# Performance work log

Hardware: AMD Instinct MI355X
Metric: run time of the kernel (lower is better)

Reference implementation:

```python
import jax, jax.numpy as jnp
import numpy as np

B, S, D, H = 2, 2048, 1024, 16
DK = D // H
LN_EPS = 1e-5


def setup_inputs() -> dict:
    key = jax.random.key(0)
    ks = jax.random.split(key, 10)
    scale = 1.0 / np.sqrt(D)
    return {
        "input_Q": jax.random.normal(ks[0], (B, S, D), jnp.float32),
        "input_K": jax.random.normal(ks[1], (B, S, D), jnp.float32),
        "input_V": jax.random.normal(ks[2], (B, S, D), jnp.float32),
        "mask": jax.random.randint(ks[3], (B, S, S), 0, 2, jnp.int32),
        "W_Q": jax.random.normal(ks[4], (D, D), jnp.float32) * scale,
        "W_K": jax.random.normal(ks[5], (D, D), jnp.float32) * scale,
        "W_V": jax.random.normal(ks[6], (D, D), jnp.float32) * scale,
        "W_O": jax.random.normal(ks[7], (D, D), jnp.float32) * scale,
        "ln_gamma": jnp.ones((D,), jnp.float32),
        "ln_beta": jnp.zeros((D,), jnp.float32),
    }


def reference(input_Q, input_K, input_V, mask, W_Q, W_K, W_V, W_O, ln_gamma, ln_beta):
    # projections -> [B, H, S, DK]
    q = (input_Q @ W_Q).reshape(B, S, H, DK).transpose(0, 2, 1, 3)
    k = (input_K @ W_K).reshape(B, S, H, DK).transpose(0, 2, 1, 3)
    v = (input_V @ W_V).reshape(B, S, H, DK).transpose(0, 2, 1, 3)

    # explicit O(S^2) scores as in the original module
    scores = jnp.einsum("bhqd,bhkd->bhqk", q, k) / np.sqrt(DK)
    scores = jnp.where(mask[:, None, :, :].astype(bool), -1e9, scores)
    attn = jax.nn.softmax(scores, axis=-1)
    ctx = jnp.einsum("bhqk,bhkd->bhqd", attn, v)

    # merge heads, output projection, residual + LayerNorm
    ctx = ctx.transpose(0, 2, 1, 3).reshape(B, S, D)
    out = ctx @ W_O + input_Q
    mu = out.mean(-1, keepdims=True)
    var = jnp.mean((out - mu) ** 2, -1, keepdims=True)
    return (out - mu) * jax.lax.rsqrt(var + LN_EPS) * ln_gamma + ln_beta
```

## Files before the change

### kernel.cpp

```cpp
#include <hip/hip_runtime.h>

typedef __bf16 bf16x8 __attribute__((ext_vector_type(8)));
typedef float  f32x4  __attribute__((ext_vector_type(4)));

#define AS1 __attribute__((address_space(1)))
#define AS3 __attribute__((address_space(3)))

__device__ __forceinline__ void g2l16(const void* g, void* l) {
  __builtin_amdgcn_global_load_lds((AS1 void*)g, (AS3 void*)l, 16, 0, 0);
}
#define MFMA16(a, b, c) __builtin_amdgcn_mfma_f32_16x16x32_bf16(a, b, c, 0, 0, 0)

__device__ __forceinline__ unsigned pack_bf16(float a, float b) {
  union { __bf16 h[2]; unsigned u; } p;
  p.h[0] = (__bf16)a; p.h[1] = (__bf16)b;
  return p.u;
}

__global__ __launch_bounds__(256) void prep(const float* __restrict__ inQ,
    const float* __restrict__ inK, const float* __restrict__ inV,
    const int* __restrict__ mask,
    const float* __restrict__ W0, const float* __restrict__ W1,
    const float* __restrict__ W2, const float* __restrict__ W3,
    __bf16* __restrict__ Xq, __bf16* __restrict__ Xk, __bf16* __restrict__ Xv,
    unsigned long long* __restrict__ bits, __bf16* __restrict__ Wt) {
  __shared__ __bf16 tile[64][65];
  const int blk = blockIdx.x;
  if (blk < 6144) {
    const int z = blk >> 11, bx = blk & 2047;
    const float* src = z == 0 ? inQ : (z == 1 ? inK : inV);
    __bf16* dst = z == 0 ? Xq : (z == 1 ? Xk : Xv);
    size_t base = ((size_t)bx * 256 + threadIdx.x) * 8;
    float4 f0 = *(const float4*)(src + base);
    float4 f1 = *(const float4*)(src + base + 4);
    bf16x8 o;
    o[0] = (__bf16)f0.x; o[1] = (__bf16)f0.y; o[2] = (__bf16)f0.z; o[3] = (__bf16)f0.w;
    o[4] = (__bf16)f1.x; o[5] = (__bf16)f1.y; o[6] = (__bf16)f1.z; o[7] = (__bf16)f1.w;
    *(bf16x8*)(dst + base) = o;
  } else if (blk < 10240) {
    const int lane = threadIdx.x & 63, w = threadIdx.x >> 6;
    const int base = (blk - 6144) * 2048 + w * 512;
#pragma unroll
    for (int it = 0; it < 8; ++it) {
      int i = base + it * 64 + lane;
      unsigned long long bb = __ballot(mask[i] != 0);
      if (lane == 0) bits[i >> 6] = bb;
    }
  } else {
    const int idx = blk - 10240;
    const int z = idx >> 8, rem = idx & 255, bx = rem & 15, by = rem >> 4;
    const float* srcs[4] = {W0, W1, W2, W3};
    const float* src = srcs[z];
    __bf16* dst = Wt + (size_t)z * 1024 * 1024;
    int cb = bx * 64, rb = by * 64;
    for (int i = threadIdx.x; i < 4096; i += 256) {
      int r = i >> 6, c = i & 63;
      tile[r][c] = (__bf16)src[(size_t)(rb + r) * 1024 + cb + c];
    }
    __syncthreads();
    for (int i = threadIdx.x; i < 4096; i += 256) {
      int c = i >> 6, r = i & 63;
      dst[(size_t)(cb + c) * 1024 + rb + r] = tile[r][c];
    }
  }
}

__global__ __launch_bounds__(256) void qkv_gemm(const __bf16* __restrict__ Xq,
    const __bf16* __restrict__ Xk, const __bf16* __restrict__ Xv,
    const __bf16* __restrict__ Wt, __bf16* __restrict__ Qb,
    __bf16* __restrict__ Kb, __bf16* __restrict__ Vtb) {
  __shared__ __align__(16) __bf16 sh[8192];
  __bf16* As = sh;
  __bf16* Bs = sh + 4096;
  const int z = blockIdx.z;
  const __bf16* X = z == 0 ? Xq : (z == 1 ? Xk : Xv);
  const __bf16* W = Wt + (size_t)z * 1048576;
  const float scale = z == 0 ? 0.125f * 1.44269504088896f : 1.f;
  const int t = threadIdx.x;
  const int lane = t & 63, w = t >> 6;
  const int lane15 = lane & 15, quad = lane >> 4;
  const int wm = (w >> 1) * 64, wn = (w & 1) * 64;
  const int mBase = blockIdx.y * 128, nBase = blockIdx.x * 128;
  const int c1 = t, c2 = t + 256;
  f32x4 acc[4][4] = {};
  for (int kt = 0; kt < 1024; kt += 32) {
    __syncthreads();
    g2l16(X + (size_t)(mBase + (c1 >> 2)) * 1024 + kt + (c1 & 3) * 8, As + c1 * 8);
    g2l16(X + (size_t)(mBase + (c2 >> 2)) * 1024 + kt + (c2 & 3) * 8, As + c2 * 8);
    g2l16(W + (size_t)(nBase + (c1 >> 2)) * 1024 + kt + (c1 & 3) * 8, Bs + c1 * 8);
    g2l16(W + (size_t)(nBase + (c2 >> 2)) * 1024 + kt + (c2 & 3) * 8, Bs + c2 * 8);
    __builtin_amdgcn_s_waitcnt(0);
    __syncthreads();
    bf16x8 a[4], b[4];
#pragma unroll
    for (int i = 0; i < 4; i++) a[i] = *(const bf16x8*)&As[(wm + i * 16 + lane15) * 32 + quad * 8];
#pragma unroll
    for (int j = 0; j < 4; j++) b[j] = *(const bf16x8*)&Bs[(wn + j * 16 + lane15) * 32 + quad * 8];
#pragma unroll
    for (int i = 0; i < 4; i++)
#pragma unroll
      for (int j = 0; j < 4; j++)
        acc[i][j] = MFMA16(a[i], b[j], acc[i][j]);
  }
  if (z != 2) {
    __bf16* Y = z == 0 ? Qb : Kb;
#pragma unroll
    for (int i = 0; i < 4; i++)
#pragma unroll
      for (int j = 0; j < 4; j++)
#pragma unroll
        for (int r = 0; r < 4; r++) {
          int mg = mBase + wm + i * 16 + quad * 4 + r;
          int ng = nBase + wn + j * 16 + lane15;
          int b_ = mg >> 11, s_ = mg & 2047, h_ = ng >> 6, d_ = ng & 63;
          Y[(((size_t)(b_ * 16 + h_)) * 2048 + s_) * 64 + d_] = (__bf16)(acc[i][j][r] * scale);
        }
  } else {
    const int s0 = mBase & 2047;
    const int bhBase = (mBase >> 11) * 16 + (nBase >> 6);
#pragma unroll
    for (int half = 0; half < 2; ++half) {
      __syncthreads();
      if ((w & 1) == half) {
#pragma unroll
        for (int i = 0; i < 4; i++)
#pragma unroll
          for (int j = 0; j < 4; j++)
#pragma unroll
            for (int r = 0; r < 4; r++) {
              int nl = j * 16 + lane15;
              int ml = wm + i * 16 + quad * 4 + r;
              sh[nl * 128 + (ml ^ ((nl & 7) * 16))] = (__bf16)acc[i][j][r];
            }
      }
      __syncthreads();
      const int row = t >> 2, c0 = (t & 3) * 32;
      const int xr = (row & 7) * 16;
      const int b0 = row * 128 + (c0 ^ xr);
      const int b1 = row * 128 + ((c0 + 16) ^ xr);
      bf16x8 a0 = *(const bf16x8*)&sh[b0];
      bf16x8 a1 = *(const bf16x8*)&sh[b0 + 8];
      bf16x8 a2 = *(const bf16x8*)&sh[b1];
      bf16x8 a3 = *(const bf16x8*)&sh[b1 + 8];
      __bf16* dst = Vtb + (size_t)(bhBase + half) * 131072 + (size_t)row * 2048 + s0 + c0;
      *(bf16x8*)(dst)      = a0;
      *(bf16x8*)(dst + 8)  = a1;
      *(bf16x8*)(dst + 16) = a2;
      *(bf16x8*)(dst + 24) = a3;
    }
  }
}

__global__ __launch_bounds__(256) void gemm_wo(const __bf16* __restrict__ X,
    const __bf16* __restrict__ Wt, const float* __restrict__ resid,
    float* __restrict__ Yf) {
  __shared__ __align__(16) __bf16 As[128 * 32];
  __shared__ __align__(16) __bf16 Bs[128 * 32];
  const int t = threadIdx.x;
  const int lane = t & 63, w = t >> 6;
  const int lane15 = lane & 15, quad = lane >> 4;
  const int wm = (w >> 1) * 64, wn = (w & 1) * 64;
  const int mBase = blockIdx.y * 128, nBase = blockIdx.x * 128;
  const int c1 = t, c2 = t + 256;
  f32x4 acc[4][4] = {};
  for (int kt = 0; kt < 1024; kt += 32) {
    __syncthreads();
    g2l16(X  + (size_t)(mBase + (c1 >> 2)) * 1024 + kt + (c1 & 3) * 8, As + c1 * 8);
    g2l16(X  + (size_t)(mBase + (c2 >> 2)) * 1024 + kt + (c2 & 3) * 8, As + c2 * 8);
    g2l16(Wt + (size_t)(nBase + (c1 >> 2)) * 1024 + kt + (c1 & 3) * 8, Bs + c1 * 8);
    g2l16(Wt + (size_t)(nBase + (c2 >> 2)) * 1024 + kt + (c2 & 3) * 8, Bs + c2 * 8);
    __builtin_amdgcn_s_waitcnt(0);
    __syncthreads();
    bf16x8 a[4], b[4];
#pragma unroll
    for (int i = 0; i < 4; i++) a[i] = *(const bf16x8*)&As[(wm + i * 16 + lane15) * 32 + quad * 8];
#pragma unroll
    for (int j = 0; j < 4; j++) b[j] = *(const bf16x8*)&Bs[(wn + j * 16 + lane15) * 32 + quad * 8];
#pragma unroll
    for (int i = 0; i < 4; i++)
#pragma unroll
      for (int j = 0; j < 4; j++)
        acc[i][j] = MFMA16(a[i], b[j], acc[i][j]);
  }
#pragma unroll
  for (int i = 0; i < 4; i++)
#pragma unroll
    for (int j = 0; j < 4; j++)
#pragma unroll
      for (int r = 0; r < 4; r++) {
        int mg = mBase + wm + i * 16 + quad * 4 + r;
        int ng = nBase + wn + j * 16 + lane15;
        size_t idx = (size_t)mg * 1024 + ng;
        Yf[idx] = acc[i][j][r] + resid[idx];
      }
}

__global__ __launch_bounds__(256) void attn_kernel(const __bf16* __restrict__ Q,
    const __bf16* __restrict__ Kp, const __bf16* __restrict__ Vt,
    const unsigned* __restrict__ mbits, __bf16* __restrict__ ctx) {
  __shared__ __align__(16) __bf16 Qs[64 * 64];
  __shared__ __align__(16) __bf16 Ks[2][32 * 64];
  __shared__ __align__(16) __bf16 Vs[2][64 * 32];
  __shared__ __align__(16) __bf16 Ps[4][16 * 32];
  const int t = threadIdx.x, lane = t & 63, w = t >> 6;
  const int l15 = lane & 15, quad = lane >> 4;
  const int bh = blockIdx.y, b = bh >> 4, h = bh & 15;
  const int qBase = blockIdx.x * 64;
  const size_t qko = (size_t)bh * 2048 * 64;
  const size_t vko = (size_t)bh * 64 * 2048;
  const int srow8 = lane >> 3, sch8 = (lane & 7) ^ srow8;
  const int srow16 = lane >> 2, sch4 = (lane & 3) ^ (srow16 & 3);
  g2l16(Q + qko + (size_t)(qBase + w * 8 + srow8) * 64 + sch8 * 8,       Qs + w * 512 + lane * 8);
  g2l16(Q + qko + (size_t)(qBase + (w + 4) * 8 + srow8) * 64 + sch8 * 8, Qs + (w + 4) * 512 + lane * 8);
  g2l16(Kp + qko + (size_t)(w * 8 + srow8) * 64 + sch8 * 8,   &Ks[0][0] + w * 512 + lane * 8);
  g2l16(Vt + vko + (size_t)(w * 16 + srow16) * 2048 + sch4 * 8, &Vs[0][0] + w * 512 + lane * 8);
  __builtin_amdgcn_s_waitcnt(0);
  __syncthreads();
  bf16x8 qb0, qb1;
  {
    const int r = w * 16 + l15, s = r & 7;
    qb0 = *(const bf16x8*)&Qs[r * 64 + ((quad ^ s) * 8)];
    qb1 = *(const bf16x8*)&Qs[r * 64 + (((4 + quad) ^ s) * 8)];
  }
  bf16x8 ones;
#pragma unroll
  for (int i = 0; i < 8; i++) ones[i] = (__bf16)1.0f;
  f32x4 o[4] = {};
  f32x4 ol = {};
  const size_t mIdx = ((size_t)b * 2048 + qBase + w * 16 + l15) * 64;
  unsigned m32 = mbits[mIdx];
  int cur = 0;
  for (int kt = 0; kt < 64; ++kt) {
    __syncthreads();
    unsigned mnext = 0;
    if (kt < 63) {
      const int tB = (kt + 1) * 32, nb = cur ^ 1;
      g2l16(Kp + qko + (size_t)(tB + w * 8 + srow8) * 64 + sch8 * 8,        &Ks[nb][0] + w * 512 + lane * 8);
      g2l16(Vt + vko + (size_t)(w * 16 + srow16) * 2048 + tB + sch4 * 8,    &Vs[nb][0] + w * 512 + lane * 8);
      mnext = mbits[mIdx + kt + 1];
    }
    f32x4 st[2];
#pragma unroll
    for (int j = 0; j < 2; j++) {
      const int tr = j * 16 + l15, s = tr & 7;
      bf16x8 ka0 = *(const bf16x8*)&Ks[cur][tr * 64 + ((quad ^ s) * 8)];
      bf16x8 ka1 = *(const bf16x8*)&Ks[cur][tr * 64 + (((4 + quad) ^ s) * 8)];
      f32x4 zz = {0.f, 0.f, 0.f, 0.f};
      zz = MFMA16(ka0, qb0, zz);
      st[j] = MFMA16(ka1, qb1, zz);
    }
#pragma unroll
    for (int j = 0; j < 2; j++) {
      const int t0 = j * 16 + quad * 4;
      float e0 = ((m32 >> (t0 + 0)) & 1u) ? 0.f : __builtin_exp2f(st[j][0]);
      float e1 = ((m32 >> (t0 + 1)) & 1u) ? 0.f : __builtin_exp2f(st[j][1]);
      float e2 = ((m32 >> (t0 + 2)) & 1u) ? 0.f : __builtin_exp2f(st[j][2]);
      float e3 = ((m32 >> (t0 + 3)) & 1u) ? 0.f : __builtin_exp2f(st[j][3]);
      const int ch = t0 >> 3;
      char* pbase = (char*)&Ps[w][0] + l15 * 64 + ((ch ^ (l15 & 3)) * 16) + ((t0 & 7) * 2);
      *(unsigned*)(pbase)     = pack_bf16(e0, e1);
      *(unsigned*)(pbase + 4) = pack_bf16(e2, e3);
    }
    m32 = mnext;
    __builtin_amdgcn_s_waitcnt(0xC07F);
    bf16x8 pa = *(const bf16x8*)&Ps[w][l15 * 32 + ((quad ^ (l15 & 3)) * 8)];
    ol = MFMA16(pa, ones, ol);
#pragma unroll
    for (int j = 0; j < 4; j++) {
      const int dr = j * 16 + l15;
      bf16x8 vb = *(const bf16x8*)&Vs[cur][dr * 32 + ((quad ^ (dr & 3)) * 8)];
      o[j] = MFMA16(pa, vb, o[j]);
    }
    cur ^= 1;
  }
#pragma unroll
  for (int r = 0; r < 4; r++) {
    float inv = 1.f / ol[r];
    int qg = qBase + w * 16 + quad * 4 + r;
    size_t base = ((size_t)b * 2048 + qg) * 1024 + h * 64;
#pragma unroll
    for (int j = 0; j < 4; j++)
      ctx[base + j * 16 + l15] = (__bf16)(o[j][r] * inv);
  }
}

__global__ __launch_bounds__(256) void ln_kernel(const float* __restrict__ X,
    const float* __restrict__ gamma, const float* __restrict__ beta,
    float* __restrict__ out) {
  __shared__ float red[8];
  const int t = threadIdx.x;
  const size_t row = blockIdx.x;
  const float* xr = X + row * 1024;
  float4 x = *(const float4*)(xr + t * 4);
  float s = x.x + x.y + x.z + x.w;
  float s2 = x.x * x.x + x.y * x.y + x.z * x.z + x.w * x.w;
#pragma unroll
  for (int off = 1; off < 64; off <<= 1) { s += __shfl_xor(s, off); s2 += __shfl_xor(s2, off); }
  if ((t & 63) == 0) { red[t >> 6] = s; red[4 + (t >> 6)] = s2; }
  __syncthreads();
  float S1 = red[0] + red[1] + red[2] + red[3];
  float S2 = red[4] + red[5] + red[6] + red[7];
  float mu = S1 * (1.f / 1024.f);
  float var = S2 * (1.f / 1024.f) - mu * mu;
  float rs = rsqrtf(var + 1e-5f);
  float4 g = *(const float4*)(gamma + t * 4);
  float4 bb = *(const float4*)(beta + t * 4);
  float4 y;
  y.x = (x.x - mu) * rs * g.x + bb.x;
  y.y = (x.y - mu) * rs * g.y + bb.y;
  y.z = (x.z - mu) * rs * g.z + bb.z;
  y.w = (x.w - mu) * rs * g.w + bb.w;
  *(float4*)(out + row * 1024 + t * 4) = y;
}

extern "C" void kernel_launch(void* const* d_in, const int* in_sizes, int n_in,
                              void* d_out, int out_size, void* d_ws, size_t ws_size,
                              hipStream_t stream) {
  const float* inQ  = (const float*)d_in[0];
  const float* inK  = (const float*)d_in[1];
  const float* inV  = (const float*)d_in[2];
  const int*   mask = (const int*)d_in[3];
  const float* WQ   = (const float*)d_in[4];
  const float* WK   = (const float*)d_in[5];
  const float* WV   = (const float*)d_in[6];
  const float* WO   = (const float*)d_in[7];
  const float* gamma = (const float*)d_in[8];
  const float* beta  = (const float*)d_in[9];

  const size_t MB = 1024 * 1024;
  char* ws = (char*)d_ws;
  __bf16* Xq  = (__bf16*)(ws);
  __bf16* Xk  = (__bf16*)(ws + 8 * MB);
  __bf16* Xv  = (__bf16*)(ws + 16 * MB);
  __bf16* Qb  = (__bf16*)(ws + 24 * MB);
  __bf16* Kb  = (__bf16*)(ws + 32 * MB);
  __bf16* Vtb = (__bf16*)(ws + 48 * MB);
  __bf16* Wt  = (__bf16*)(ws + 56 * MB);
  unsigned long long* mbits = (unsigned long long*)(ws + 64 * MB);
  __bf16* ctx  = Xq;
  float*  outp = (float*)(ws + 8 * MB);

  prep<<<dim3(11264), 256, 0, stream>>>(inQ, inK, inV, mask, WQ, WK, WV, WO,
                                        Xq, Xk, Xv, mbits, Wt);
  qkv_gemm<<<dim3(8, 32, 3), 256, 0, stream>>>(Xq, Xk, Xv, Wt, Qb, Kb, Vtb);
  attn_kernel<<<dim3(32, 32), 256, 0, stream>>>(Qb, Kb, Vtb, (const unsigned*)mbits, ctx);
  gemm_wo<<<dim3(8, 32), 256, 0, stream>>>(ctx, Wt + 3 * 1048576, inQ, outp);
  ln_kernel<<<dim3(4096), 256, 0, stream>>>(outp, gamma, beta, (float*)d_out);
}
```

Baseline: 317.1 us.

## Use additive float mask in attention, retile Wo GEMM, adjust LDS swizzles

The prep kernel now expands the int mask into a float additive mask (0 or -1e9) instead of a packed bitmask. Attention adds it to scores before exp2, removing per-element bit tests and selects. gemm_wo moves to 64x128 tiles for twice as many blocks, and the V and P LDS swizzles change to reduce bank conflicts. The float mask costs much more memory traffic than the bitmask, per head and in prep.

Measured after the change: 316.3 us. Within noise of the previous version (-0.3%).

```diff
diff --git a/kernel.cpp b/kernel.cpp
--- a/kernel.cpp
+++ b/kernel.cpp
@@ -23,7 +23,7 @@
     const float* __restrict__ W0, const float* __restrict__ W1,
     const float* __restrict__ W2, const float* __restrict__ W3,
     __bf16* __restrict__ Xq, __bf16* __restrict__ Xk, __bf16* __restrict__ Xv,
-    unsigned long long* __restrict__ bits, __bf16* __restrict__ Wt) {
+    float* __restrict__ Mf, __bf16* __restrict__ Wt) {
   __shared__ __bf16 tile[64][65];
   const int blk = blockIdx.x;
   if (blk < 6144) {
@@ -38,14 +38,16 @@
     o[4] = (__bf16)f1.x; o[5] = (__bf16)f1.y; o[6] = (__bf16)f1.z; o[7] = (__bf16)f1.w;
     *(bf16x8*)(dst + base) = o;
   } else if (blk < 10240) {
-    const int lane = threadIdx.x & 63, w = threadIdx.x >> 6;
-    const int base = (blk - 6144) * 2048 + w * 512;
-#pragma unroll
-    for (int it = 0; it < 8; ++it) {
-      int i = base + it * 64 + lane;
-      unsigned long long bb = __ballot(mask[i] != 0);
-      if (lane == 0) bits[i >> 6] = bb;
-    }
+    size_t base = ((size_t)(blk - 6144) * 2048) + (size_t)threadIdx.x * 8;
+    int4 m0 = *(const int4*)(mask + base);
+    int4 m1 = *(const int4*)(mask + base + 4);
+    float4 f0, f1;
+    f0.x = m0.x ? -1e9f : 0.f; f0.y = m0.y ? -1e9f : 0.f;
+    f0.z = m0.z ? -1e9f : 0.f; f0.w = m0.w ? -1e9f : 0.f;
+    f1.x = m1.x ? -1e9f : 0.f; f1.y = m1.y ? -1e9f : 0.f;
+    f1.z = m1.z ? -1e9f : 0.f; f1.w = m1.w ? -1e9f : 0.f;
+    *(float4*)(Mf + base) = f0;
+    *(float4*)(Mf + base + 4) = f1;
   } else {
     const int idx = blk - 10240;
     const int z = idx >> 8, rem = idx & 255, bx = rem & 15, by = rem >> 4;
@@ -154,36 +156,34 @@
 __global__ __launch_bounds__(256) void gemm_wo(const __bf16* __restrict__ X,
     const __bf16* __restrict__ Wt, const float* __restrict__ resid,
     float* __restrict__ Yf) {
-  __shared__ __align__(16) __bf16 As[128 * 32];
+  __shared__ __align__(16) __bf16 As[64 * 32];
   __shared__ __align__(16) __bf16 Bs[128 * 32];
   const int t = threadIdx.x;
   const int lane = t & 63, w = t >> 6;
   const int lane15 = lane & 15, quad = lane >> 4;
-  const int wm = (w >> 1) * 64, wn = (w & 1) * 64;
-  const int mBase = blockIdx.y * 128, nBase = blockIdx.x * 128;
-  const int c1 = t, c2 = t + 256;
-  f32x4 acc[4][4] = {};
+  const int wm = (w >> 1) * 32, wn = (w & 1) * 64;
+  const int mBase = blockIdx.y * 64, nBase = blockIdx.x * 128;
+  f32x4 acc[2][4] = {};
   for (int kt = 0; kt < 1024; kt += 32) {
     __syncthreads();
-    g2l16(X  + (size_t)(mBase + (c1 >> 2)) * 1024 + kt + (c1 & 3) * 8, As + c1 * 8);
-    g2l16(X  + (size_t)(mBase + (c2 >> 2)) * 1024 + kt + (c2 & 3) * 8, As + c2 * 8);
-    g2l16(Wt + (size_t)(nBase + (c1 >> 2)) * 1024 + kt + (c1 & 3) * 8, Bs + c1 * 8);
-    g2l16(Wt + (size_t)(nBase + (c2 >> 2)) * 1024 + kt + (c2 & 3) * 8, Bs + c2 * 8);
+    g2l16(X  + (size_t)(mBase + (t >> 2)) * 1024 + kt + (t & 3) * 8, As + t * 8);
+    g2l16(Wt + (size_t)(nBase + (t >> 2)) * 1024 + kt + (t & 3) * 8, Bs + t * 8);
+    g2l16(Wt + (size_t)(nBase + ((t + 256) >> 2)) * 1024 + kt + (t & 3) * 8, Bs + (t + 256) * 8);
     __builtin_amdgcn_s_waitcnt(0);
     __syncthreads();
-    bf16x8 a[4], b[4];
-#pragma unroll
-    for (int i = 0; i < 4; i++) a[i] = *(const bf16x8*)&As[(wm + i * 16 + lane15) * 32 + quad * 8];
+    bf16x8 a[2], b[4];
+#pragma unroll
+    for (int i = 0; i < 2; i++) a[i] = *(const bf16x8*)&As[(wm + i * 16 + lane15) * 32 + quad * 8];
 #pragma unroll
     for (int j = 0; j < 4; j++) b[j] = *(const bf16x8*)&Bs[(wn + j * 16 + lane15) * 32 + quad * 8];
 #pragma unroll
-    for (int i = 0; i < 4; i++)
+    for (int i = 0; i < 2; i++)
 #pragma unroll
       for (int j = 0; j < 4; j++)
         acc[i][j] = MFMA16(a[i], b[j], acc[i][j]);
   }
 #pragma unroll
-  for (int i = 0; i < 4; i++)
+  for (int i = 0; i < 2; i++)
 #pragma unroll
     for (int j = 0; j < 4; j++)
 #pragma unroll
@@ -197,7 +197,7 @@
 
 __global__ __launch_bounds__(256) void attn_kernel(const __bf16* __restrict__ Q,
     const __bf16* __restrict__ Kp, const __bf16* __restrict__ Vt,
-    const unsigned* __restrict__ mbits, __bf16* __restrict__ ctx) {
+    const float* __restrict__ Mf, __bf16* __restrict__ ctx) {
   __shared__ __align__(16) __bf16 Qs[64 * 64];
   __shared__ __align__(16) __bf16 Ks[2][32 * 64];
   __shared__ __align__(16) __bf16 Vs[2][64 * 32];
@@ -209,11 +209,15 @@
   const size_t qko = (size_t)bh * 2048 * 64;
   const size_t vko = (size_t)bh * 64 * 2048;
   const int srow8 = lane >> 3, sch8 = (lane & 7) ^ srow8;
-  const int srow16 = lane >> 2, sch4 = (lane & 3) ^ (srow16 & 3);
+  const int srow16 = lane >> 2, sch4 = (lane & 3) ^ ((lane >> 3) & 3);
+  const int psw = (l15 >> 1) & 3;
   g2l16(Q + qko + (size_t)(qBase + w * 8 + srow8) * 64 + sch8 * 8,       Qs + w * 512 + lane * 8);
   g2l16(Q + qko + (size_t)(qBase + (w + 4) * 8 + srow8) * 64 + sch8 * 8, Qs + (w + 4) * 512 + lane * 8);
-  g2l16(Kp + qko + (size_t)(w * 8 + srow8) * 64 + sch8 * 8,   &Ks[0][0] + w * 512 + lane * 8);
+  g2l16(Kp + qko + (size_t)(w * 8 + srow8) * 64 + sch8 * 8,     &Ks[0][0] + w * 512 + lane * 8);
   g2l16(Vt + vko + (size_t)(w * 16 + srow16) * 2048 + sch4 * 8, &Vs[0][0] + w * 512 + lane * 8);
+  const float* Mrow = Mf + ((size_t)b * 2048 + qBase + w * 16 + l15) * 2048 + quad * 4;
+  float4 mc0 = *(const float4*)(Mrow);
+  float4 mc1 = *(const float4*)(Mrow + 16);
   __builtin_amdgcn_s_waitcnt(0);
   __syncthreads();
   bf16x8 qb0, qb1;
@@ -227,17 +231,16 @@
   for (int i = 0; i < 8; i++) ones[i] = (__bf16)1.0f;
   f32x4 o[4] = {};
   f32x4 ol = {};
-  const size_t mIdx = ((size_t)b * 2048 + qBase + w * 16 + l15) * 64;
-  unsigned m32 = mbits[mIdx];
   int cur = 0;
   for (int kt = 0; kt < 64; ++kt) {
     __syncthreads();
-    unsigned mnext = 0;
+    float4 mn0, mn1;
     if (kt < 63) {
       const int tB = (kt + 1) * 32, nb = cur ^ 1;
-      g2l16(Kp + qko + (size_t)(tB + w * 8 + srow8) * 64 + sch8 * 8,        &Ks[nb][0] + w * 512 + lane * 8);
-      g2l16(Vt + vko + (size_t)(w * 16 + srow16) * 2048 + tB + sch4 * 8,    &Vs[nb][0] + w * 512 + lane * 8);
-      mnext = mbits[mIdx + kt + 1];
+      g2l16(Kp + qko + (size_t)(tB + w * 8 + srow8) * 64 + sch8 * 8,     &Ks[nb][0] + w * 512 + lane * 8);
+      g2l16(Vt + vko + (size_t)(w * 16 + srow16) * 2048 + tB + sch4 * 8, &Vs[nb][0] + w * 512 + lane * 8);
+      mn0 = *(const float4*)(Mrow + tB);
+      mn1 = *(const float4*)(Mrow + tB + 16);
     }
     f32x4 st[2];
 #pragma unroll
@@ -251,24 +254,25 @@
     }
 #pragma unroll
     for (int j = 0; j < 2; j++) {
+      const float4 mv = j == 0 ? mc0 : mc1;
+      float e0 = __builtin_exp2f(st[j][0] + mv.x);
+      float e1 = __builtin_exp2f(st[j][1] + mv.y);
+      float e2 = __builtin_exp2f(st[j][2] + mv.z);
+      float e3 = __builtin_exp2f(st[j][3] + mv.w);
       const int t0 = j * 16 + quad * 4;
-      float e0 = ((m32 >> (t0 + 0)) & 1u) ? 0.f : __builtin_exp2f(st[j][0]);
-      float e1 = ((m32 >> (t0 + 1)) & 1u) ? 0.f : __builtin_exp2f(st[j][1]);
-      float e2 = ((m32 >> (t0 + 2)) & 1u) ? 0.f : __builtin_exp2f(st[j][2]);
-      float e3 = ((m32 >> (t0 + 3)) & 1u) ? 0.f : __builtin_exp2f(st[j][3]);
       const int ch = t0 >> 3;
-      char* pbase = (char*)&Ps[w][0] + l15 * 64 + ((ch ^ (l15 & 3)) * 16) + ((t0 & 7) * 2);
+      char* pbase = (char*)&Ps[w][0] + l15 * 64 + ((ch ^ psw) * 16) + ((t0 & 7) * 2);
       *(unsigned*)(pbase)     = pack_bf16(e0, e1);
       *(unsigned*)(pbase + 4) = pack_bf16(e2, e3);
     }
-    m32 = mnext;
+    mc0 = mn0; mc1 = mn1;
     __builtin_amdgcn_s_waitcnt(0xC07F);
-    bf16x8 pa = *(const bf16x8*)&Ps[w][l15 * 32 + ((quad ^ (l15 & 3)) * 8)];
+    bf16x8 pa = *(const bf16x8*)&Ps[w][l15 * 32 + ((quad ^ psw) * 8)];
     ol = MFMA16(pa, ones, ol);
 #pragma unroll
     for (int j = 0; j < 4; j++) {
       const int dr = j * 16 + l15;
-      bf16x8 vb = *(const bf16x8*)&Vs[cur][dr * 32 + ((quad ^ (dr & 3)) * 8)];
+      bf16x8 vb = *(const bf16x8*)&Vs[cur][dr * 32 + ((quad ^ ((dr >> 1) & 3)) * 8)];
       o[j] = MFMA16(pa, vb, o[j]);
     }
     cur ^= 1;
@@ -336,14 +340,14 @@
   __bf16* Kb  = (__bf16*)(ws + 32 * MB);
   __bf16* Vtb = (__bf16*)(ws + 48 * MB);
   __bf16* Wt  = (__bf16*)(ws + 56 * MB);
-  unsigned long long* mbits = (unsigned long long*)(ws + 64 * MB);
+  float*  Mf  = (float*)(ws + 66 * MB);
   __bf16* ctx  = Xq;
   float*  outp = (float*)(ws + 8 * MB);
 
   prep<<<dim3(11264), 256, 0, stream>>>(inQ, inK, inV, mask, WQ, WK, WV, WO,
-                                        Xq, Xk, Xv, mbits, Wt);
+                                        Xq, Xk, Xv, Mf, Wt);
   qkv_gemm<<<dim3(8, 32, 3), 256, 0, stream>>>(Xq, Xk, Xv, Wt, Qb, Kb, Vtb);
-  attn_kernel<<<dim3(32, 32), 256, 0, stream>>>(Qb, Kb, Vtb, (const unsigned*)mbits, ctx);
-  gemm_wo<<<dim3(8, 32), 256, 0, stream>>>(ctx, Wt + 3 * 1048576, inQ, outp);
+  attn_kernel<<<dim3(32, 32), 256, 0, stream>>>(Qb, Kb, Vtb, Mf, ctx);
+  gemm_wo<<<dim3(8, 64), 256, 0, stream>>>(ctx, Wt + 3 * 1048576, inQ, outp);
   ln_kernel<<<dim3(4096), 256, 0, stream>>>(outp, gamma, beta, (float*)d_out);
 }
```

## Software-pipeline attention PV stage and halve output-projection GEMM M-tile

Applied to the files above, without the earlier changes.

The attention loop now defers each tile's P·V MFMAs by one iteration, so the QK^T MFMAs of tile kt overlap with the P·V of tile kt-1. To support this it uses a 4-deep V buffer and a double-buffered P scratch per wave, and changes the LDS swizzle for V and P. Separately, gemm_wo drops to 64x128 tiles and launches twice as many blocks, which gives 512 blocks across the CUs but less reuse of the B tile. The extra LDS may lower attention occupancy, and the new swizzles have to stay consistent between writer and reader.

Result: faster. 308.4 us (-2.8%).

```diff
diff --git a/kernel.cpp b/kernel.cpp
--- a/kernel.cpp
+++ b/kernel.cpp
@@ -154,36 +154,34 @@
 __global__ __launch_bounds__(256) void gemm_wo(const __bf16* __restrict__ X,
     const __bf16* __restrict__ Wt, const float* __restrict__ resid,
     float* __restrict__ Yf) {
-  __shared__ __align__(16) __bf16 As[128 * 32];
+  __shared__ __align__(16) __bf16 As[64 * 32];
   __shared__ __align__(16) __bf16 Bs[128 * 32];
   const int t = threadIdx.x;
   const int lane = t & 63, w = t >> 6;
   const int lane15 = lane & 15, quad = lane >> 4;
-  const int wm = (w >> 1) * 64, wn = (w & 1) * 64;
-  const int mBase = blockIdx.y * 128, nBase = blockIdx.x * 128;
-  const int c1 = t, c2 = t + 256;
-  f32x4 acc[4][4] = {};
+  const int wm = (w >> 1) * 32, wn = (w & 1) * 64;
+  const int mBase = blockIdx.y * 64, nBase = blockIdx.x * 128;
+  f32x4 acc[2][4] = {};
   for (int kt = 0; kt < 1024; kt += 32) {
     __syncthreads();
-    g2l16(X  + (size_t)(mBase + (c1 >> 2)) * 1024 + kt + (c1 & 3) * 8, As + c1 * 8);
-    g2l16(X  + (size_t)(mBase + (c2 >> 2)) * 1024 + kt + (c2 & 3) * 8, As + c2 * 8);
-    g2l16(Wt + (size_t)(nBase + (c1 >> 2)) * 1024 + kt + (c1 & 3) * 8, Bs + c1 * 8);
-    g2l16(Wt + (size_t)(nBase + (c2 >> 2)) * 1024 + kt + (c2 & 3) * 8, Bs + c2 * 8);
+    g2l16(X  + (size_t)(mBase + (t >> 2)) * 1024 + kt + (t & 3) * 8, As + t * 8);
+    g2l16(Wt + (size_t)(nBase + (t >> 2)) * 1024 + kt + (t & 3) * 8, Bs + t * 8);
+    g2l16(Wt + (size_t)(nBase + ((t + 256) >> 2)) * 1024 + kt + (t & 3) * 8, Bs + (t + 256) * 8);
     __builtin_amdgcn_s_waitcnt(0);
     __syncthreads();
-    bf16x8 a[4], b[4];
-#pragma unroll
-    for (int i = 0; i < 4; i++) a[i] = *(const bf16x8*)&As[(wm + i * 16 + lane15) * 32 + quad * 8];
+    bf16x8 a[2], b[4];
+#pragma unroll
+    for (int i = 0; i < 2; i++) a[i] = *(const bf16x8*)&As[(wm + i * 16 + lane15) * 32 + quad * 8];
 #pragma unroll
     for (int j = 0; j < 4; j++) b[j] = *(const bf16x8*)&Bs[(wn + j * 16 + lane15) * 32 + quad * 8];
 #pragma unroll
-    for (int i = 0; i < 4; i++)
+    for (int i = 0; i < 2; i++)
 #pragma unroll
       for (int j = 0; j < 4; j++)
         acc[i][j] = MFMA16(a[i], b[j], acc[i][j]);
   }
 #pragma unroll
-  for (int i = 0; i < 4; i++)
+  for (int i = 0; i < 2; i++)
 #pragma unroll
     for (int j = 0; j < 4; j++)
 #pragma unroll
@@ -200,20 +198,23 @@
     const unsigned* __restrict__ mbits, __bf16* __restrict__ ctx) {
   __shared__ __align__(16) __bf16 Qs[64 * 64];
   __shared__ __align__(16) __bf16 Ks[2][32 * 64];
-  __shared__ __align__(16) __bf16 Vs[2][64 * 32];
-  __shared__ __align__(16) __bf16 Ps[4][16 * 32];
+  __shared__ __align__(16) __bf16 Vs[4][64 * 32];
+  __shared__ __align__(16) __bf16 Ps[4][2][16 * 32];
   const int t = threadIdx.x, lane = t & 63, w = t >> 6;
   const int l15 = lane & 15, quad = lane >> 4;
+  const int psw = (l15 >> 1) & 3;
   const int bh = blockIdx.y, b = bh >> 4, h = bh & 15;
   const int qBase = blockIdx.x * 64;
   const size_t qko = (size_t)bh * 2048 * 64;
   const size_t vko = (size_t)bh * 64 * 2048;
   const int srow8 = lane >> 3, sch8 = (lane & 7) ^ srow8;
-  const int srow16 = lane >> 2, sch4 = (lane & 3) ^ (srow16 & 3);
+  const int srow16 = lane >> 2, sch4 = (lane & 3) ^ ((lane >> 3) & 3);
   g2l16(Q + qko + (size_t)(qBase + w * 8 + srow8) * 64 + sch8 * 8,       Qs + w * 512 + lane * 8);
   g2l16(Q + qko + (size_t)(qBase + (w + 4) * 8 + srow8) * 64 + sch8 * 8, Qs + (w + 4) * 512 + lane * 8);
-  g2l16(Kp + qko + (size_t)(w * 8 + srow8) * 64 + sch8 * 8,   &Ks[0][0] + w * 512 + lane * 8);
+  g2l16(Kp + qko + (size_t)(w * 8 + srow8) * 64 + sch8 * 8,     &Ks[0][0] + w * 512 + lane * 8);
   g2l16(Vt + vko + (size_t)(w * 16 + srow16) * 2048 + sch4 * 8, &Vs[0][0] + w * 512 + lane * 8);
+  const size_t mIdx = ((size_t)b * 2048 + qBase + w * 16 + l15) * 64;
+  unsigned m32 = mbits[mIdx];
   __builtin_amdgcn_s_waitcnt(0);
   __syncthreads();
   bf16x8 qb0, qb1;
@@ -227,28 +228,38 @@
   for (int i = 0; i < 8; i++) ones[i] = (__bf16)1.0f;
   f32x4 o[4] = {};
   f32x4 ol = {};
-  const size_t mIdx = ((size_t)b * 2048 + qBase + w * 16 + l15) * 64;
-  unsigned m32 = mbits[mIdx];
-  int cur = 0;
+  bf16x8 pa_prev;
+#pragma unroll 4
   for (int kt = 0; kt < 64; ++kt) {
     __syncthreads();
     unsigned mnext = 0;
     if (kt < 63) {
-      const int tB = (kt + 1) * 32, nb = cur ^ 1;
-      g2l16(Kp + qko + (size_t)(tB + w * 8 + srow8) * 64 + sch8 * 8,        &Ks[nb][0] + w * 512 + lane * 8);
-      g2l16(Vt + vko + (size_t)(w * 16 + srow16) * 2048 + tB + sch4 * 8,    &Vs[nb][0] + w * 512 + lane * 8);
+      const int tB = (kt + 1) * 32;
+      g2l16(Kp + qko + (size_t)(tB + w * 8 + srow8) * 64 + sch8 * 8,     &Ks[(kt + 1) & 1][0] + w * 512 + lane * 8);
+      g2l16(Vt + vko + (size_t)(w * 16 + srow16) * 2048 + tB + sch4 * 8, &Vs[(kt + 1) & 3][0] + w * 512 + lane * 8);
       mnext = mbits[mIdx + kt + 1];
     }
     f32x4 st[2];
 #pragma unroll
     for (int j = 0; j < 2; j++) {
       const int tr = j * 16 + l15, s = tr & 7;
-      bf16x8 ka0 = *(const bf16x8*)&Ks[cur][tr * 64 + ((quad ^ s) * 8)];
-      bf16x8 ka1 = *(const bf16x8*)&Ks[cur][tr * 64 + (((4 + quad) ^ s) * 8)];
+      bf16x8 ka0 = *(const bf16x8*)&Ks[kt & 1][tr * 64 + ((quad ^ s) * 8)];
+      bf16x8 ka1 = *(const bf16x8*)&Ks[kt & 1][tr * 64 + (((4 + quad) ^ s) * 8)];
       f32x4 zz = {0.f, 0.f, 0.f, 0.f};
       zz = MFMA16(ka0, qb0, zz);
       st[j] = MFMA16(ka1, qb1, zz);
     }
+    if (kt > 0) {
+      const __bf16* Vb = &Vs[(kt - 1) & 3][0];
+      ol = MFMA16(pa_prev, ones, ol);
+#pragma unroll
+      for (int j = 0; j < 4; j++) {
+        const int dr = j * 16 + l15;
+        bf16x8 vb = *(const bf16x8*)&Vb[dr * 32 + ((quad ^ ((dr >> 1) & 3)) * 8)];
+        o[j] = MFMA16(pa_prev, vb, o[j]);
+      }
+    }
+    __bf16* Pw = &Ps[w][kt & 1][0];
 #pragma unroll
     for (int j = 0; j < 2; j++) {
       const int t0 = j * 16 + quad * 4;
@@ -257,21 +268,23 @@
       float e2 = ((m32 >> (t0 + 2)) & 1u) ? 0.f : __builtin_exp2f(st[j][2]);
       float e3 = ((m32 >> (t0 + 3)) & 1u) ? 0.f : __builtin_exp2f(st[j][3]);
       const int ch = t0 >> 3;
-      char* pbase = (char*)&Ps[w][0] + l15 * 64 + ((ch ^ (l15 & 3)) * 16) + ((t0 & 7) * 2);
+      char* pbase = (char*)Pw + l15 * 64 + ((ch ^ psw) * 16) + ((t0 & 7) * 2);
       *(unsigned*)(pbase)     = pack_bf16(e0, e1);
       *(unsigned*)(pbase + 4) = pack_bf16(e2, e3);
     }
     m32 = mnext;
     __builtin_amdgcn_s_waitcnt(0xC07F);
-    bf16x8 pa = *(const bf16x8*)&Ps[w][l15 * 32 + ((quad ^ (l15 & 3)) * 8)];
-    ol = MFMA16(pa, ones, ol);
+    pa_prev = *(const bf16x8*)&Pw[l15 * 32 + ((quad ^ psw) * 8)];
+  }
+  {
+    const __bf16* Vb = &Vs[63 & 3][0];
+    ol = MFMA16(pa_prev, ones, ol);
 #pragma unroll
     for (int j = 0; j < 4; j++) {
       const int dr = j * 16 + l15;
-      bf16x8 vb = *(const bf16x8*)&Vs[cur][dr * 32 + ((quad ^ (dr & 3)) * 8)];
-      o[j] = MFMA16(pa, vb, o[j]);
-    }
-    cur ^= 1;
+      bf16x8 vb = *(const bf16x8*)&Vb[dr * 32 + ((quad ^ ((dr >> 1) & 3)) * 8)];
+      o[j] = MFMA16(pa_prev, vb, o[j]);
+    }
   }
 #pragma unroll
   for (int r = 0; r < 4; r++) {
@@ -344,6 +357,6 @@
                                         Xq, Xk, Xv, mbits, Wt);
   qkv_gemm<<<dim3(8, 32, 3), 256, 0, stream>>>(Xq, Xk, Xv, Wt, Qb, Kb, Vtb);
   attn_kernel<<<dim3(32, 32), 256, 0, stream>>>(Qb, Kb, Vtb, (const unsigned*)mbits, ctx);
-  gemm_wo<<<dim3(8, 32), 256, 0, stream>>>(ctx, Wt + 3 * 1048576, inQ, outp);
+  gemm_wo<<<dim3(8, 64), 256, 0, stream>>>(ctx, Wt + 3 * 1048576, inQ, outp);
   ln_kernel<<<dim3(4096), 256, 0, stream>>>(outp, gamma, beta, (float*)d_out);
 }
```
